# Performance work log

Hardware: AMD Instinct MI355X
Metric: run time of the kernel (lower is better)

## Reference

```python
import jax, jax.numpy as jnp
import numpy as np

NUM_CLASSES = 13
HIDDEN = 64
NUM_LAYERS = 2
NODE_FEAT = 1 + 4 + NUM_CLASSES  # 18
N_NODES = 100000
N_EDGES = 1600000


def _glorot(key, shape):
    fan_in, fan_out = shape[0], shape[1]
    lim = (6.0 / (fan_in + fan_out)) ** 0.5
    return jax.random.uniform(key, shape, jnp.float32, -lim, lim)


def setup_inputs() -> dict:
    key = jax.random.key(0)
    ks = jax.random.split(key, 32)
    H = HIDDEN
    inp = {
        "node_features": jax.random.normal(ks[0], (N_NODES, NODE_FEAT), jnp.float32),
        "edge_index": jax.random.randint(ks[1], (2, N_EDGES), 0, N_NODES, jnp.int32),
        "edge_weights": jax.random.uniform(ks[2], (N_EDGES,), jnp.float32),
        "embed_W": _glorot(ks[3], (NODE_FEAT, H)),
        "embed_b": jnp.zeros((H,), jnp.float32),
        # stacked per-layer params, leading dim = NUM_LAYERS
        "msg_W1": jnp.stack([_glorot(ks[4 + i], (2 * H, H)) for i in range(NUM_LAYERS)]),
        "msg_b1": jnp.zeros((NUM_LAYERS, H), jnp.float32),
        "msg_W2": jnp.stack([_glorot(ks[8 + i], (H, H)) for i in range(NUM_LAYERS)]),
        "msg_b2": jnp.zeros((NUM_LAYERS, H), jnp.float32),
        "att_W1": jnp.stack([_glorot(ks[12 + i], (2 * H, H // 2)) for i in range(NUM_LAYERS)]),
        "att_b1": jnp.zeros((NUM_LAYERS, H // 2), jnp.float32),
        "att_W2": jnp.stack([_glorot(ks[16 + i], (H // 2, 1)) for i in range(NUM_LAYERS)]),
        "att_b2": jnp.zeros((NUM_LAYERS, 1), jnp.float32),
        "upd_W1": jnp.stack([_glorot(ks[20 + i], (2 * H, H)) for i in range(NUM_LAYERS)]),
        "upd_b1": jnp.zeros((NUM_LAYERS, H), jnp.float32),
        "upd_W2": jnp.stack([_glorot(ks[24 + i], (H, H)) for i in range(NUM_LAYERS)]),
        "upd_b2": jnp.zeros((NUM_LAYERS, H), jnp.float32),
        "head_W": _glorot(ks[28], (H, 1)),
        "head_b": jnp.zeros((1,), jnp.float32),
    }
    return inp


def _mlp2(x, W1, b1, W2, b2):
    return jax.nn.relu(x @ W1 + b1) @ W2 + b2


def reference(node_features, edge_index, edge_weights,
              embed_W, embed_b,
              msg_W1, msg_b1, msg_W2, msg_b2,
              att_W1, att_b1, att_W2, att_b2,
              upd_W1, upd_b1, upd_W2, upd_b2,
              head_W, head_b):
    row, col = edge_index[0], edge_index[1]
    x = jax.nn.relu(node_features @ embed_W + embed_b)  # [N, H]
    num_nodes = x.shape[0]
    for l in range(NUM_LAYERS):
        cat = jnp.concatenate([x[row], x[col]], axis=-1)  # [E, 2H]
        messages = _mlp2(cat, msg_W1[l], msg_b1[l], msg_W2[l], msg_b2[l])  # [E, H]
        att = jax.nn.sigmoid(_mlp2(cat, att_W1[l], att_b1[l], att_W2[l], att_b2[l])[:, 0])  # [E]
        fw = edge_weights * att
        messages = messages * fw[:, None]
        aggregated = jax.ops.segment_sum(messages, col, num_segments=num_nodes)  # [N, H]
        norm = jax.ops.segment_sum(fw, col, num_segments=num_nodes)
        norm = jnp.clip(norm, 1e-6, None)
        aggregated = aggregated / norm[:, None]
        x_new = _mlp2(jnp.concatenate([x, aggregated], axis=-1),
                      upd_W1[l], upd_b1[l], upd_W2[l], upd_b2[l])
        x = jax.nn.relu(x_new + x)
    series_repr = jnp.max(x, axis=0)  # [H]
    binary_logit = (series_repr @ head_W + head_b)[0]
    return binary_logit
```

## Files before the change

### kernel.cpp

```cpp
#include <hip/hip_runtime.h>
#include <hip/hip_bf16.h>
#include <math.h>

#define H 64
#define F 18
#define NPW 8
#define NBKT 1024
#define EPB 8192

typedef _Float16 f16x8 __attribute__((ext_vector_type(8)));
typedef _Float16 f16x4 __attribute__((ext_vector_type(4)));
typedef float f32x4 __attribute__((ext_vector_type(4)));

__global__ __launch_bounds__(256) void embed_kernel(
    const float* __restrict__ nf, const float* __restrict__ W,
    const float* __restrict__ b, _Float16* __restrict__ xh, int N)
{
    int n = blockIdx.x * 256 + threadIdx.x;
    if (n >= N) return;
    float acc[H];
#pragma unroll
    for (int j = 0; j < H; ++j) acc[j] = b[j];
    const float* f = nf + (long)n * F;
#pragma unroll
    for (int i = 0; i < F; ++i) {
        float c = f[i];
        const float* w = W + i * H;
#pragma unroll
        for (int j = 0; j < H; ++j) acc[j] += c * w[j];
    }
    union { uint4 v[8]; _Float16 h[64]; } O;
#pragma unroll
    for (int j = 0; j < H; ++j) O.h[j] = (_Float16)fmaxf(acc[j], 0.f);
    uint4* xo = (uint4*)(xh + (size_t)n * H);
#pragma unroll
    for (int i = 0; i < 8; ++i) xo[i] = O.v[i];
}

__global__ __launch_bounds__(256) void packfrag_uv_kernel(
    const float* __restrict__ mW1, const float* __restrict__ aW1,
    f16x8* __restrict__ uvB)
{
    int t = blockIdx.x * 256 + threadIdx.x;
    if (t >= 3072) return;
    int lane = t & 63;
    int frag = t >> 6;
    int l = frag / 24, rem = frag % 24;
    int side = rem / 12, q = rem % 12;
    int nt = q >> 1, kk = q & 1;
    int quad = lane >> 4, l15 = lane & 15;
    int col = nt * 16 + l15;
    f16x8 v;
#pragma unroll
    for (int j = 0; j < 8; ++j) {
        int k = side * 64 + kk * 32 + quad * 8 + j;
        float w = (col < 64) ? mW1[(size_t)l * 8192 + k * 64 + col]
                             : aW1[(size_t)l * 4096 + k * 32 + (col - 64)];
        v[j] = (_Float16)w;
    }
    uvB[(size_t)frag * 64 + lane] = v;
}

__global__ __launch_bounds__(256) void prep_update_kernel(
    const float* __restrict__ mW2, const float* __restrict__ mb2,
    const float* __restrict__ uW1,
    float* __restrict__ M2U, float* __restrict__ mbu)
{
    int t = blockIdx.x * 256 + threadIdx.x;
    if (t >= 2 * 64 * 64) return;
    int l = t >> 12, r = t & 4095;
    int i = r >> 6, j = r & 63;
    const float* W2 = mW2 + (size_t)l * 4096;
    const float* U1b = uW1 + (size_t)l * 8192 + 4096;
    float s = 0.f;
    for (int k = 0; k < 64; ++k) s += W2[i * 64 + k] * U1b[k * 64 + j];
    M2U[t] = s;
    if (i == 0) {
        float sb = 0.f;
        const float* b2 = mb2 + (size_t)l * 64;
        for (int k = 0; k < 64; ++k) sb += b2[k] * U1b[k * 64 + j];
        mbu[l * 64 + j] = sb;
    }
}

__global__ __launch_bounds__(256) void packfrag_upd_kernel(
    const float* __restrict__ uW1, const float* __restrict__ M2U,
    const float* __restrict__ uW2, f16x8* __restrict__ updB)
{
    int t = blockIdx.x * 256 + threadIdx.x;
    if (t >= 3072) return;
    int lane = t & 63;
    int frag = t >> 6;
    int l = frag / 24, f = frag % 24;
    int quad = lane >> 4, l15 = lane & 15;
    int g = f >> 3, ff = f & 7;
    int nt = ff >> 1, kk = ff & 1;
    const float* src;
    if (g == 0)      src = uW1 + (size_t)l * 8192;
    else if (g == 1) src = M2U + (size_t)l * 4096;
    else             src = uW2 + (size_t)l * 4096;
    f16x8 v;
#pragma unroll
    for (int j = 0; j < 8; ++j) {
        int k = kk * 32 + quad * 8 + j;
        v[j] = (_Float16)src[k * 64 + nt * 16 + l15];
    }
    updB[(size_t)frag * 64 + lane] = v;
}

__global__ __launch_bounds__(256) void scan1_kernel(
    const int* __restrict__ deg, int* __restrict__ part,
    int* __restrict__ bsum, int N)
{
    __shared__ int lds[256];
    int t = threadIdx.x;
    int base = blockIdx.x * 1024 + t * 4;
    int v[4];
#pragma unroll
    for (int s = 0; s < 4; ++s) v[s] = (base + s < N) ? deg[base + s] : 0;
    int sum = v[0] + v[1] + v[2] + v[3];
    lds[t] = sum;
    __syncthreads();
    for (int off = 1; off < 256; off <<= 1) {
        int xv = (t >= off) ? lds[t - off] : 0;
        __syncthreads();
        lds[t] += xv;
        __syncthreads();
    }
    int excl = lds[t] - sum;
    if (t == 255) bsum[blockIdx.x] = lds[255];
    int p = excl;
#pragma unroll
    for (int s = 0; s < 4; ++s) {
        if (base + s < N) part[base + s] = p;
        p += v[s];
    }
}

__global__ __launch_bounds__(256) void scan2_kernel(int* __restrict__ bsum, int nb)
{
    __shared__ int lds[256];
    int t = threadIdx.x;
    int v = (t < nb) ? bsum[t] : 0;
    lds[t] = v;
    __syncthreads();
    for (int off = 1; off < 256; off <<= 1) {
        int xv = (t >= off) ? lds[t - off] : 0;
        __syncthreads();
        lds[t] += xv;
        __syncthreads();
    }
    if (t < nb) bsum[t] = lds[t] - v;
}

__global__ __launch_bounds__(256) void scan3_kernel(
    int* __restrict__ part, const int* __restrict__ bsum, int N)
{
    int i = blockIdx.x * 256 + threadIdx.x;
    if (i >= N) return;
    part[i] = part[i] + bsum[i >> 10];
}

__global__ __launch_bounds__(256) void count_bucket_kernel(
    const int* __restrict__ col, int* __restrict__ cnt,
    int E, int NB, int NBK, int BS)
{
    __shared__ int lc[NBKT];
    int t = threadIdx.x;
    for (int i = t; i < NBK; i += 256) lc[i] = 0;
    __syncthreads();
    for (int s = 0; s < EPB / 256; ++s) {
        int e = blockIdx.x * EPB + s * 256 + t;
        if (e < E) atomicAdd(lc + (unsigned)col[e] / (unsigned)BS, 1);
    }
    __syncthreads();
    for (int i = t; i < NBK; i += 256)
        cnt[(size_t)i * NB + blockIdx.x] = lc[i];
}

__global__ __launch_bounds__(256) void place_kernel(
    const int* __restrict__ row, const int* __restrict__ col,
    const float* __restrict__ ew, const int* __restrict__ off,
    int2* __restrict__ edata, int E, int NB, int NBK, int BS)
{
    __shared__ int lc[NBKT];
    int t = threadIdx.x;
    for (int i = t; i < NBK; i += 256) lc[i] = 0;
    __syncthreads();
    for (int s = 0; s < EPB / 256; ++s) {
        int e = blockIdx.x * EPB + s * 256 + t;
        if (e < E) {
            int cv = col[e];
            int c = (unsigned)cv / (unsigned)BS;
            int lcol = cv - c * BS;
            int r = atomicAdd(lc + c, 1);
            int pos = off[(size_t)c * NB + blockIdx.x] + r;
            edata[pos] = make_int2(row[e] | (lcol << 20), __float_as_int(ew[e]));
        }
    }
}

__global__ __launch_bounds__(256) void bucket_sort_kernel(
    int2* __restrict__ edata, const int* __restrict__ off,
    int* __restrict__ deg, int* __restrict__ startp,
    int NB, int BS, int N, int E, int NBK)
{
    __shared__ int hist[256];
    __shared__ int psum[256];
    int b = blockIdx.x;
    int t = threadIdx.x;
    int base = off[(size_t)b * NB];
    int end  = (b + 1 < NBK) ? off[(size_t)(b + 1) * NB] : E;
    int cnt = end - base;
    int nlo = b * BS;

    hist[t] = 0;
    __syncthreads();

    int2 regs[8];
    int lnode[8];
#pragma unroll
    for (int ii = 0; ii < 8; ++ii) {
        int i = t + ii * 256;
        if (i < cnt) {
            regs[ii] = edata[base + i];
            lnode[ii] = ((unsigned)regs[ii].x) >> 20;
            atomicAdd(hist + lnode[ii], 1);
        }
    }
    __syncthreads();

    int cv = hist[t];
    psum[t] = cv;
    __syncthreads();
    for (int o = 1; o < 256; o <<= 1) {
        int xv = (t >= o) ? psum[t - o] : 0;
        __syncthreads();
        psum[t] += xv;
        __syncthreads();
    }
    int excl = psum[t] - cv;
    int ng = nlo + t;
    if (t < BS && ng < N) {
        deg[ng] = cv;
        startp[ng] = base + excl;
    }
    hist[t] = excl;
    __syncthreads();

#pragma unroll
    for (int ii = 0; ii < 8; ++ii) {
        int i = t + ii * 256;
        if (i < cnt) {
            int pos = atomicAdd(hist + lnode[ii], 1);
            edata[base + pos] = make_int2(regs[ii].x & 0xFFFFF, regs[ii].y);
        }
    }
}

__global__ __launch_bounds__(256) void uv_mfma_kernel(
    const _Float16* __restrict__ xh, const f16x8* __restrict__ Bf,
    const float* __restrict__ mb1, const float* __restrict__ ab1,
    _Float16* __restrict__ out, int N, int side)
{
    int lane = threadIdx.x & 63;
    int wid = (blockIdx.x * 256 + threadIdx.x) >> 6;
    int quad = lane >> 4, l15 = lane & 15;
    int nbase = wid * 64;
    if (nbase >= N) return;

    f16x8 B[12];
#pragma unroll
    for (int i = 0; i < 12; ++i) B[i] = Bf[i * 64 + lane];
    float bv[6];
#pragma unroll
    for (int nt = 0; nt < 6; ++nt) {
        int col = nt * 16 + l15;
        bv[nt] = side ? 0.f : (col < 64 ? mb1[col] : ab1[col - 64]);
    }

    for (int mt = 0; mt < 4; ++mt) {
        int na = nbase + mt * 16 + l15;
        if (na >= N) na = N - 1;
        const f16x8* xrow = (const f16x8*)(xh + (size_t)na * H);
        f16x8 Ax[2];
        Ax[0] = xrow[quad];
        Ax[1] = xrow[4 + quad];

        f32x4 C[6];
#pragma unroll
        for (int nt = 0; nt < 6; ++nt) {
            f32x4 cc = {bv[nt], bv[nt], bv[nt], bv[nt]};
#pragma unroll
            for (int kk = 0; kk < 2; ++kk)
                cc = __builtin_amdgcn_mfma_f32_16x16x32_f16(Ax[kk], B[nt * 2 + kk], cc, 0, 0, 0);
            C[nt] = cc;
        }
#pragma unroll
        for (int r = 0; r < 4; ++r) {
            int n = nbase + mt * 16 + quad * 4 + r;
            if (n < N) {
#pragma unroll
                for (int nt = 0; nt < 6; ++nt)
                    out[(size_t)n * 96 + nt * 16 + l15] = (_Float16)C[nt][r];
            }
        }
    }
}

__global__ __launch_bounds__(256) void edge_gather_kernel(
    const _Float16* __restrict__ Ur,
    const _Float16* __restrict__ Vc,
    const int2* __restrict__ edata,
    const int* __restrict__ startp, const int* __restrict__ deg,
    const float* __restrict__ aW2, const float* __restrict__ ab2,
    _Float16* __restrict__ aggN, float* __restrict__ snorm, int N)
{
    int wid = (blockIdx.x * 256 + threadIdx.x) >> 6;
    int lane = threadIdx.x & 63;
    int g = lane >> 3, s = lane & 7;
    int n0 = wid * NPW;
    if (n0 >= N) return;
    int n1 = n0 + NPW; if (n1 > N) n1 = N;

    float aw2v[4];
#pragma unroll
    for (int j = 0; j < 4; ++j) aw2v[j] = aW2[s * 4 + j];
    float ab2v = ab2[0];

    for (int n = n0; n < n1; ++n) {
        int e0 = startp[n];
        int d = deg[n];
        const _Float16* vrow = Vc + (size_t)n * 96;
        f16x8 vm = *(const f16x8*)(vrow + s * 8);
        f16x4 va = *(const f16x4*)(vrow + 64 + s * 4);

        float acc[8];
#pragma unroll
        for (int j = 0; j < 8; ++j) acc[j] = 0.f;
        float rfw = 0.f;

        int iters = (d + 7) >> 3;
        for (int it = 0; it < iters; ++it) {
            int ei = it * 8 + g;
            bool valid = ei < d;
            int e = e0 + (valid ? ei : 0);
            int2 ed = edata[e];
            float ew = valid ? __int_as_float(ed.y) : 0.f;
            const _Float16* urow = Ur + (size_t)ed.x * 96;
            f16x8 um = *(const f16x8*)(urow + s * 8);
            f16x4 ua = *(const f16x4*)(urow + 64 + s * 4);

            _Float16 h[8];
#pragma unroll
            for (int j = 0; j < 8; ++j) {
                _Float16 z = um[j] + vm[j];
                h[j] = z > (_Float16)0 ? z : (_Float16)0;
            }
            float pp = 0.f;
#pragma unroll
            for (int j = 0; j < 4; ++j) {
                _Float16 za = ua[j] + va[j];
                float zf = (float)(za > (_Float16)0 ? za : (_Float16)0);
                pp += zf * aw2v[j];
            }
            pp += __shfl_xor(pp, 1);
            pp += __shfl_xor(pp, 2);
            pp += __shfl_xor(pp, 4);
            float fw = ew / (1.f + __expf(-(pp + ab2v)));
#pragma unroll
            for (int j = 0; j < 8; ++j) acc[j] += (float)h[j] * fw;
            rfw += fw;
        }

#pragma unroll
        for (int o = 8; o <= 32; o <<= 1) {
#pragma unroll
            for (int j = 0; j < 8; ++j) acc[j] += __shfl_xor(acc[j], o);
            rfw += __shfl_xor(rfw, o);
        }
        float inv = 1.f / fmaxf(rfw, 1e-6f);
        if (g == 0) {
            union { _Float16 h[8]; uint4 v; } O;
#pragma unroll
            for (int j = 0; j < 8; ++j) O.h[j] = (_Float16)(acc[j] * inv);
            *(uint4*)(aggN + (size_t)n * H + s * 8) = O.v;
        }
        if (lane == 0) snorm[n] = rfw * inv;
    }
}

__global__ __launch_bounds__(256, 2) void update_mfma_kernel(
    _Float16* __restrict__ xh, const _Float16* __restrict__ agg,
    const float* __restrict__ snorm,
    const f16x8* __restrict__ Bfrag,
    const float* __restrict__ mbu,
    const float* __restrict__ ub1, const float* __restrict__ ub2, int N)
{
    __shared__ __align__(16) _Float16 hlds[4][16 * 80];
    int wib = threadIdx.x >> 6;
    int lane = threadIdx.x & 63;
    int wid = (blockIdx.x * 256 + threadIdx.x) >> 6;
    int quad = lane >> 4, l15 = lane & 15;
    int nbase = wid * 64;
    if (nbase >= N) return;

    f16x8 Bu[8], Bm[8], Bw[8];
#pragma unroll
    for (int i = 0; i < 8; ++i) {
        Bu[i] = Bfrag[i * 64 + lane];
        Bm[i] = Bfrag[(8 + i) * 64 + lane];
        Bw[i] = Bfrag[(16 + i) * 64 + lane];
    }
    float mbuv[4], b1v[4], b2v[4];
#pragma unroll
    for (int nt = 0; nt < 4; ++nt) {
        mbuv[nt] = mbu[nt * 16 + l15];
        b1v[nt] = ub1[nt * 16 + l15];
        b2v[nt] = ub2[nt * 16 + l15];
    }

    for (int mt = 0; mt < 4; ++mt) {
        int na = nbase + mt * 16 + l15;
        if (na >= N) na = N - 1;
        const f16x8* xrow = (const f16x8*)(xh + (size_t)na * H);
        f16x8 Ax[2];
        Ax[0] = xrow[quad];
        Ax[1] = xrow[4 + quad];
        const f16x8* arow = (const f16x8*)(agg + (size_t)na * H);
        f16x8 Aa[2];
        Aa[0] = arow[quad];
        Aa[1] = arow[4 + quad];

        f32x4 Cx[4], Ca[4];
#pragma unroll
        for (int nt = 0; nt < 4; ++nt) {
            f32x4 cx = {0.f, 0.f, 0.f, 0.f}, ca = {0.f, 0.f, 0.f, 0.f};
#pragma unroll
            for (int kk = 0; kk < 2; ++kk) {
                cx = __builtin_amdgcn_mfma_f32_16x16x32_f16(Ax[kk], Bu[nt * 2 + kk], cx, 0, 0, 0);
                ca = __builtin_amdgcn_mfma_f32_16x16x32_f16(Aa[kk], Bm[nt * 2 + kk], ca, 0, 0, 0);
            }
            Cx[nt] = cx; Ca[nt] = ca;
        }

        int noder = nbase + mt * 16 + quad * 4;
        float sn_r[4];
#pragma unroll
        for (int r = 0; r < 4; ++r) {
            int ng = noder + r; if (ng >= N) ng = N - 1;
            sn_r[r] = snorm[ng];
        }

#pragma unroll
        for (int nt = 0; nt < 4; ++nt) {
#pragma unroll
            for (int r = 0; r < 4; ++r) {
                float hv = fmaxf(Cx[nt][r] + Ca[nt][r]
                                 + sn_r[r] * mbuv[nt] + b1v[nt], 0.f);
                hlds[wib][(quad * 4 + r) * 80 + nt * 16 + l15] = (_Float16)hv;
            }
        }
        __asm__ __volatile__("s_waitcnt lgkmcnt(0)" ::: "memory");
        f16x8 Ah[2];
        Ah[0] = *(const f16x8*)&hlds[wib][l15 * 80 + quad * 8];
        Ah[1] = *(const f16x8*)&hlds[wib][l15 * 80 + 32 + quad * 8];
        __asm__ __volatile__("s_waitcnt lgkmcnt(0)" ::: "memory");

        f32x4 C2[4];
#pragma unroll
        for (int nt = 0; nt < 4; ++nt) {
            f32x4 cc = {0.f, 0.f, 0.f, 0.f};
#pragma unroll
            for (int kk = 0; kk < 2; ++kk)
                cc = __builtin_amdgcn_mfma_f32_16x16x32_f16(Ah[kk], Bw[nt * 2 + kk], cc, 0, 0, 0);
            C2[nt] = cc;
        }

#pragma unroll
        for (int r = 0; r < 4; ++r) {
            int ng = noder + r;
            if (ng < N) {
#pragma unroll
                for (int nt = 0; nt < 4; ++nt) {
                    size_t idx = (size_t)ng * H + nt * 16 + l15;
                    float xo = (float)xh[idx];
                    xh[idx] = (_Float16)fmaxf(C2[nt][r] + b2v[nt] + xo, 0.f);
                }
            }
        }
    }
}

__global__ __launch_bounds__(256) void max_kernel(
    const _Float16* __restrict__ xh16, unsigned int* __restrict__ serp, int N)
{
    int j = threadIdx.x & (H - 1);
    int g = (blockIdx.x * 256 + threadIdx.x) >> 6;
    int stride = (gridDim.x * 256) >> 6;
    float m = 0.f;
    for (int n = g; n < N; n += stride)
        m = fmaxf(m, (float)xh16[(size_t)n * H + j]);
    atomicMax(serp + j, __float_as_uint(m));
}

__global__ void head_kernel(const unsigned int* __restrict__ serp,
                            const float* __restrict__ hW,
                            const float* __restrict__ hb,
                            float* __restrict__ out)
{
    int j = threadIdx.x;
    float v = __uint_as_float(serp[j]) * hW[j];
#pragma unroll
    for (int off = 32; off > 0; off >>= 1) v += __shfl_down(v, off);
    if (j == 0) out[0] = v + hb[0];
}

extern "C" void kernel_launch(void* const* d_in, const int* in_sizes, int n_in,
                              void* d_out, int out_size, void* d_ws, size_t ws_size,
                              hipStream_t stream)
{
    const float* nf  = (const float*)d_in[0];
    const int*   ei  = (const int*)d_in[1];
    const float* ew  = (const float*)d_in[2];
    const float* eW  = (const float*)d_in[3];
    const float* eb_ = (const float*)d_in[4];
    const float* mW1 = (const float*)d_in[5];
    const float* mb1 = (const float*)d_in[6];
    const float* mW2 = (const float*)d_in[7];
    const float* mb2 = (const float*)d_in[8];
    const float* aW1 = (const float*)d_in[9];
    const float* ab1 = (const float*)d_in[10];
    const float* aW2 = (const float*)d_in[11];
    const float* ab2 = (const float*)d_in[12];
    const float* uW1 = (const float*)d_in[13];
    const float* ub1 = (const float*)d_in[14];
    const float* uW2 = (const float*)d_in[15];
    const float* ub2 = (const float*)d_in[16];
    const float* hW  = (const float*)d_in[17];
    const float* hb  = (const float*)d_in[18];

    int N = in_sizes[0] / F;
    int E = in_sizes[2];
    const int* row = ei;
    const int* col = ei + E;

    size_t Nr = ((size_t)N + 3) & ~(size_t)3;
    size_t Er = ((size_t)E + 3) & ~(size_t)3;

    int BS  = (N + NBKT - 1) / NBKT;
    int NBK = (N + BS - 1) / BS;
    int NB  = (E + EPB - 1) / EPB;
    size_t M  = (size_t)NBK * NB;
    size_t Mr = (M + 3) & ~(size_t)3;

    _Float16* xh   = (_Float16*)d_ws;
    _Float16* aggN = xh + Nr * 64;
    float* snorm   = (float*)(aggN + Nr * 64);
    unsigned int* serp = (unsigned int*)(snorm + Nr);
    int* deg       = (int*)(serp + 64);
    int* startp    = deg + Nr;
    int* bsum      = startp + Nr;
    float* M2U     = (float*)(bsum + 256);
    float* mbu     = M2U + 8192;
    f16x8* updB    = (f16x8*)(mbu + 128);
    f16x8* uvB     = updB + 3072;
    _Float16* Ur   = (_Float16*)(uvB + 3072);
    _Float16* Vc   = Ur + Nr * 96;
    int* cnt       = (int*)(Vc + Nr * 96);
    int* off       = cnt + Mr;
    int2* edata    = (int2*)(off + Mr);

    int nb_n = (N + 255) / 256;
    int nbA = (int)((M + 1023) / 1024);

    count_bucket_kernel<<<NB, 256, 0, stream>>>(col, cnt, E, NB, NBK, BS);
    scan1_kernel<<<nbA, 256, 0, stream>>>(cnt, off, bsum, (int)M);
    scan2_kernel<<<1, 256, 0, stream>>>(bsum, nbA);
    scan3_kernel<<<(int)((M + 255) / 256), 256, 0, stream>>>(off, bsum, (int)M);
    place_kernel<<<NB, 256, 0, stream>>>(row, col, ew, off, edata, E, NB, NBK, BS);
    bucket_sort_kernel<<<NBK, 256, 0, stream>>>(edata, off, deg, startp,
                                                NB, BS, N, E, NBK);

    packfrag_uv_kernel<<<12, 256, 0, stream>>>(mW1, aW1, uvB);
    prep_update_kernel<<<32, 256, 0, stream>>>(mW2, mb2, uW1, M2U, mbu);
    packfrag_upd_kernel<<<12, 256, 0, stream>>>(uW1, M2U, uW2, updB);
    embed_kernel<<<nb_n, 256, 0, stream>>>(nf, eW, eb_, xh, N);

    int nwaves_n = (N + 63) / 64;
    int nb_uv = (N + 255) / 256;
    int nb_eg = (N + NPW * 4 - 1) / (NPW * 4);
    for (int l = 0; l < 2; ++l) {
        uv_mfma_kernel<<<nb_uv, 256, 0, stream>>>(
            xh, uvB + ((size_t)l * 2 + 0) * 12 * 64,
            mb1 + (size_t)l * H, ab1 + (size_t)l * (H / 2), Ur, N, 0);
        uv_mfma_kernel<<<nb_uv, 256, 0, stream>>>(
            xh, uvB + ((size_t)l * 2 + 1) * 12 * 64,
            mb1, ab1, Vc, N, 1);
        edge_gather_kernel<<<nb_eg, 256, 0, stream>>>(
            Ur, Vc, edata, startp, deg,
            aW2 + (size_t)l * (H / 2), ab2 + (size_t)l,
            aggN, snorm, N);
        update_mfma_kernel<<<(nwaves_n + 3) / 4, 256, 0, stream>>>(
            xh, aggN, snorm,
            updB + (size_t)l * 24 * 64,
            mbu + (size_t)l * 64,
            ub1 + (size_t)l * H, ub2 + (size_t)l * H, N);
    }

    hipMemsetAsync(serp, 0, 64 * sizeof(unsigned int), stream);
    max_kernel<<<256, 256, 0, stream>>>(xh, serp, N);
    head_kernel<<<1, 64, 0, stream>>>(serp, hW, hb, (float*)d_out);
}
```

Measured before the change: 415.7 us.

## Merge U/V launches, interleave UV buffer, and software-pipeline edge gathers

```diff
diff --git a/kernel.cpp b/kernel.cpp
--- a/kernel.cpp
+++ b/kernel.cpp
@@ -4,7 +4,7 @@
 
 #define H 64
 #define F 18
-#define NPW 8
+#define NPW 16
 #define NBKT 1024
 #define EPB 8192
 
@@ -261,17 +261,21 @@
 __global__ __launch_bounds__(256) void uv_mfma_kernel(
     const _Float16* __restrict__ xh, const f16x8* __restrict__ Bf,
     const float* __restrict__ mb1, const float* __restrict__ ab1,
-    _Float16* __restrict__ out, int N, int side)
-{
+    _Float16* __restrict__ UV, int N, int nbside)
+{
+    int bid = blockIdx.x;
+    int side = (bid >= nbside) ? 1 : 0;
+    int b = bid - side * nbside;
     int lane = threadIdx.x & 63;
-    int wid = (blockIdx.x * 256 + threadIdx.x) >> 6;
+    int wid = (b * 256 + (int)threadIdx.x) >> 6;
     int quad = lane >> 4, l15 = lane & 15;
     int nbase = wid * 64;
     if (nbase >= N) return;
 
+    const f16x8* Bs = Bf + side * 12 * 64;
     f16x8 B[12];
 #pragma unroll
-    for (int i = 0; i < 12; ++i) B[i] = Bf[i * 64 + lane];
+    for (int i = 0; i < 12; ++i) B[i] = Bs[i * 64 + lane];
     float bv[6];
 #pragma unroll
     for (int nt = 0; nt < 6; ++nt) {
@@ -302,15 +306,14 @@
             if (n < N) {
 #pragma unroll
                 for (int nt = 0; nt < 6; ++nt)
-                    out[(size_t)n * 96 + nt * 16 + l15] = (_Float16)C[nt][r];
+                    UV[(size_t)n * 192 + side * 96 + nt * 16 + l15] = (_Float16)C[nt][r];
             }
         }
     }
 }
 
 __global__ __launch_bounds__(256) void edge_gather_kernel(
-    const _Float16* __restrict__ Ur,
-    const _Float16* __restrict__ Vc,
+    const _Float16* __restrict__ UV,
     const int2* __restrict__ edata,
     const int* __restrict__ startp, const int* __restrict__ deg,
     const float* __restrict__ aW2, const float* __restrict__ ab2,
@@ -331,7 +334,8 @@
     for (int n = n0; n < n1; ++n) {
         int e0 = startp[n];
         int d = deg[n];
-        const _Float16* vrow = Vc + (size_t)n * 96;
+        int iters = (d + 7) >> 3;
+        const _Float16* vrow = UV + (size_t)n * 192 + 96;
         f16x8 vm = *(const f16x8*)(vrow + s * 8);
         f16x4 va = *(const f16x4*)(vrow + 64 + s * 4);
 
@@ -340,37 +344,57 @@
         for (int j = 0; j < 8; ++j) acc[j] = 0.f;
         float rfw = 0.f;
 
-        int iters = (d + 7) >> 3;
-        for (int it = 0; it < iters; ++it) {
-            int ei = it * 8 + g;
-            bool valid = ei < d;
-            int e = e0 + (valid ? ei : 0);
-            int2 ed = edata[e];
-            float ew = valid ? __int_as_float(ed.y) : 0.f;
-            const _Float16* urow = Ur + (size_t)ed.x * 96;
-            f16x8 um = *(const f16x8*)(urow + s * 8);
-            f16x4 ua = *(const f16x4*)(urow + 64 + s * 4);
-
-            _Float16 h[8];
-#pragma unroll
-            for (int j = 0; j < 8; ++j) {
-                _Float16 z = um[j] + vm[j];
-                h[j] = z > (_Float16)0 ? z : (_Float16)0;
+        if (iters > 0) {
+            int2 ed0, ed1 = {0, 0}, ed2 = {0, 0};
+            f16x8 um0;
+            f16x4 ua0;
+            {
+                int ei = g;
+                ed0 = edata[e0 + (ei < d ? ei : 0)];
+                const _Float16* ur = UV + (size_t)ed0.x * 192;
+                um0 = *(const f16x8*)(ur + s * 8);
+                ua0 = *(const f16x4*)(ur + 64 + s * 4);
             }
-            float pp = 0.f;
-#pragma unroll
-            for (int j = 0; j < 4; ++j) {
-                _Float16 za = ua[j] + va[j];
-                float zf = (float)(za > (_Float16)0 ? za : (_Float16)0);
-                pp += zf * aw2v[j];
+            if (iters > 1) {
+                int ei = 8 + g;
+                ed1 = edata[e0 + (ei < d ? ei : 0)];
             }
-            pp += __shfl_xor(pp, 1);
-            pp += __shfl_xor(pp, 2);
-            pp += __shfl_xor(pp, 4);
-            float fw = ew / (1.f + __expf(-(pp + ab2v)));
-#pragma unroll
-            for (int j = 0; j < 8; ++j) acc[j] += (float)h[j] * fw;
-            rfw += fw;
+            for (int it = 0; it < iters; ++it) {
+                f16x8 umn = um0;
+                f16x4 uan = ua0;
+                if (it + 1 < iters) {
+                    const _Float16* ur = UV + (size_t)ed1.x * 192;
+                    umn = *(const f16x8*)(ur + s * 8);
+                    uan = *(const f16x4*)(ur + 64 + s * 4);
+                }
+                if (it + 2 < iters) {
+                    int ei = (it + 2) * 8 + g;
+                    ed2 = edata[e0 + (ei < d ? ei : 0)];
+                }
+
+                int ei = it * 8 + g;
+                float ew = (ei < d) ? __int_as_float(ed0.y) : 0.f;
+                float pp = 0.f;
+#pragma unroll
+                for (int j = 0; j < 4; ++j) {
+                    _Float16 za = ua0[j] + va[j];
+                    za = za > (_Float16)0 ? za : (_Float16)0;
+                    pp += (float)za * aw2v[j];
+                }
+                pp += __shfl_xor(pp, 1);
+                pp += __shfl_xor(pp, 2);
+                pp += __shfl_xor(pp, 4);
+                float fw = ew / (1.f + __expf(-(pp + ab2v)));
+#pragma unroll
+                for (int j = 0; j < 8; ++j) {
+                    _Float16 z = um0[j] + vm[j];
+                    z = z > (_Float16)0 ? z : (_Float16)0;
+                    acc[j] += (float)z * fw;
+                }
+                rfw += fw;
+
+                ed0 = ed1; ed1 = ed2; um0 = umn; ua0 = uan;
+            }
         }
 
 #pragma unroll
@@ -565,9 +589,8 @@
     float* mbu     = M2U + 8192;
     f16x8* updB    = (f16x8*)(mbu + 128);
     f16x8* uvB     = updB + 3072;
-    _Float16* Ur   = (_Float16*)(uvB + 3072);
-    _Float16* Vc   = Ur + Nr * 96;
-    int* cnt       = (int*)(Vc + Nr * 96);
+    _Float16* UV   = (_Float16*)(uvB + 3072);
+    int* cnt       = (int*)(UV + Nr * 192);
     int* off       = cnt + Mr;
     int2* edata    = (int2*)(off + Mr);
 
@@ -591,14 +614,11 @@
     int nb_uv = (N + 255) / 256;
     int nb_eg = (N + NPW * 4 - 1) / (NPW * 4);
     for (int l = 0; l < 2; ++l) {
-        uv_mfma_kernel<<<nb_uv, 256, 0, stream>>>(
-            xh, uvB + ((size_t)l * 2 + 0) * 12 * 64,
-            mb1 + (size_t)l * H, ab1 + (size_t)l * (H / 2), Ur, N, 0);
-        uv_mfma_kernel<<<nb_uv, 256, 0, stream>>>(
-            xh, uvB + ((size_t)l * 2 + 1) * 12 * 64,
-            mb1, ab1, Vc, N, 1);
+        uv_mfma_kernel<<<2 * nb_uv, 256, 0, stream>>>(
+            xh, uvB + (size_t)l * 24 * 64,
+            mb1 + (size_t)l * H, ab1 + (size_t)l * (H / 2), UV, N, nb_uv);
         edge_gather_kernel<<<nb_eg, 256, 0, stream>>>(
-            Ur, Vc, edata, startp, deg,
+            UV, edata, startp, deg,
             aW2 + (size_t)l * (H / 2), ab2 + (size_t)l,
             aggN, snorm, N);
         update_mfma_kernel<<<(nwaves_n + 3) / 4, 256, 0, stream>>>(
```

After: 420.9 us. Within noise of the previous version (+1.3%).
